# Optimization experiments

Hardware: AMD Instinct MI355X
Metric: run time of the kernel (lower is better)

## Reference

```python
import jax, jax.numpy as jnp
import numpy as np

N_NODES = 20000
N_EDGES = 5000
STEPS = 50
INFECTION_RATE = 0.01
RECOVERY_RATE = 0.038
EDGE_DENSITY = 0.002  # ~10 hyperedges per node on average


def setup_inputs() -> dict:
    key = jax.random.key(0)
    k1, k2 = jax.random.split(key, 2)
    # initial SIR state per node: valid probability rows summing to 1
    u = jax.random.uniform(k1, (N_NODES, 3), dtype=jnp.float32)
    x = u / u.sum(axis=1, keepdims=True)
    # binary hypergraph incidence matrix (num_hyperedges, num_nodes)
    H = (jax.random.uniform(k2, (N_EDGES, N_NODES)) < EDGE_DENSITY).astype(jnp.float32)
    beta = jnp.full((N_NODES,), INFECTION_RATE, dtype=jnp.float32)
    gamma = jnp.full((N_NODES,), RECOVERY_RATE, dtype=jnp.float32)
    return {"x": x, "H": H, "beta": beta, "gamma": gamma, "steps": STEPS}


def reference(x, H, beta, gamma, steps):
    # x: (N, 3) [S, I, R] per node; H: (E, N) incidence.
    def step(state, _):
        S, I, R = state[:, 0], state[:, 1], state[:, 2]
        # hypergraph message passing: node -> hyperedge -> node
        new_cases = beta * (S * (H.T @ (H @ I)))
        new_recovery = gamma * I
        nxt = jnp.stack(
            [S - new_cases, I + new_cases - new_recovery, R + new_recovery], axis=1
        )
        nxt = jnp.maximum(nxt, 0.0)                       # clamp(min=0)
        nxt = nxt / nxt.sum(axis=1, keepdims=True)        # per-node row normalize
        return nxt, nxt

    _, traj = jax.lax.scan(step, x, None, length=steps - 1)
    # output[0] = initial state, then steps-1 simulated updates -> (steps, N, 3)
    return jnp.concatenate([x[None], traj], axis=0)
```

## Files before the change

kernel.cpp:

```cpp
#include <hip/hip_runtime.h>


#define EDGE_CAP 96
#define NODE_CAP 32
#define NIDX_REG 16
#define COOP_BLOCKS 128
#define COOP_THREADS 1024
#define NFLAGS 128

typedef unsigned int uint4_ev __attribute__((ext_vector_type(4)));

__global__ void zero_counts_kernel(int* edge_cnt, int* node_cnt, unsigned* flags,
                                   int n_edges, int n_nodes) {
    int i = blockIdx.x * blockDim.x + threadIdx.x;
    if (i < NFLAGS) flags[i] = 0u;
    if (i < n_edges) edge_cnt[i] = 0;
    if (i < n_nodes) node_cnt[i] = 0;
}

__global__ void build_adjacency_kernel(const float* __restrict__ H,
                                       int* __restrict__ edge_cnt,
                                       int* __restrict__ edge_nodes,
                                       int* __restrict__ node_cnt,
                                       int* __restrict__ node_edges,
                                       int n_nodes) {
    __shared__ int cnt;
    __shared__ int cols[EDGE_CAP];
    __shared__ unsigned long long qmask[128];
    const int e  = blockIdx.x;
    const int tx = threadIdx.x;
    if (tx == 0) cnt = 0;
    const float* row = H + (size_t)e * n_nodes;
    const uint4_ev* row4 = (const uint4_ev*)row;
    const int n4 = n_nodes >> 2;
    const int niter = (n4 + 255) >> 8;

    for (int i = 0; i < niter; ++i) {
        int q = (i << 8) + tx;
        uint4_ev v = {0u, 0u, 0u, 0u};
        if (q < n4) v = row4[q];
        unsigned long long m = __ballot((v.x | v.y | v.z | v.w) != 0u);
        if ((tx & 63) == 0) qmask[(i << 2) + (tx >> 6)] = m;
    }
    __syncthreads();

    const int nslots = niter << 2;
    for (int sIdx = tx; sIdx < nslots; sIdx += blockDim.x) {
        unsigned long long m = qmask[sIdx];
        int qbase = ((sIdx >> 2) << 8) + ((sIdx & 3) << 6);
        while (m) {
            int lane = __builtin_ctzll(m); m &= m - 1;
            int q = qbase + lane;
            uint4_ev v = row4[q];
            int cbase = q << 2;
            if (v.x) { int p = atomicAdd(&cnt, 1); if (p < EDGE_CAP) cols[p] = cbase; }
            if (v.y) { int p = atomicAdd(&cnt, 1); if (p < EDGE_CAP) cols[p] = cbase + 1; }
            if (v.z) { int p = atomicAdd(&cnt, 1); if (p < EDGE_CAP) cols[p] = cbase + 2; }
            if (v.w) { int p = atomicAdd(&cnt, 1); if (p < EDGE_CAP) cols[p] = cbase + 3; }
        }
    }
    if (tx == 0) {
        for (int c = n4 << 2; c < n_nodes; ++c)
            if (row[c] != 0.0f) { int p = atomicAdd(&cnt, 1); if (p < EDGE_CAP) cols[p] = c; }
    }
    __syncthreads();

    int cn = min(cnt, EDGE_CAP);
    if (tx == 0) edge_cnt[e] = cn;
    for (int i = tx; i < cn; i += blockDim.x) {
        int c = cols[i];
        edge_nodes[e * EDGE_CAP + i] = c;
        int q = atomicAdd(&node_cnt[c], 1);
        if (q < NODE_CAP) node_edges[c * NODE_CAP + q] = e;
    }
}

__device__ __forceinline__ float coh_load(const float* p) {
    return __hip_atomic_load(p, __ATOMIC_RELAXED, __HIP_MEMORY_SCOPE_AGENT);
}
__device__ __forceinline__ void coh_storef(float* p, float v) {
    __hip_atomic_store(p, v, __ATOMIC_RELAXED, __HIP_MEMORY_SCOPE_AGENT);
}
__device__ __forceinline__ unsigned coh_loadu(const unsigned* p) {
    return __hip_atomic_load(p, __ATOMIC_RELAXED, __HIP_MEMORY_SCOPE_AGENT);
}
__device__ __forceinline__ void coh_storeu(unsigned* p, unsigned v) {
    __hip_atomic_store(p, v, __ATOMIC_RELAXED, __HIP_MEMORY_SCOPE_AGENT);
}

__device__ __forceinline__ void bar_pub(unsigned* flags, unsigned ph) {
    asm volatile("s_waitcnt vmcnt(0)" ::: "memory");
    __syncthreads();
    if (threadIdx.x == 0) coh_storeu(&flags[blockIdx.x], ph);
}
__device__ __forceinline__ void bar_poll(unsigned* flags, unsigned ph) {
    if (threadIdx.x < 64) {
        for (;;) {
            unsigned a = coh_loadu(&flags[threadIdx.x]);
            unsigned b = coh_loadu(&flags[64 + threadIdx.x]);
            if (__ballot((a < ph) || (b < ph)) == 0ull) break;
            __builtin_amdgcn_s_sleep(1);
        }
    }
    __syncthreads();
    asm volatile("" ::: "memory");
}

__global__ __launch_bounds__(COOP_THREADS) void sir_steps_kernel(
        const float* __restrict__ x,
        const int* __restrict__ edge_cnt, const int* __restrict__ edge_nodes,
        const int* __restrict__ node_cnt, const int* __restrict__ node_edges,
        const float* __restrict__ beta, const float* __restrict__ gamma,
        float* __restrict__ y, float* __restrict__ I,
        float* __restrict__ out,
        int n_nodes, int n_edges, int steps, unsigned* flags) {
    const int b  = blockIdx.x;
    const int tx = threadIdx.x;

    const int node_chunk = (n_nodes + gridDim.x - 1) / gridDim.x;
    const int edge_chunk = (n_edges + gridDim.x - 1) / gridDim.x;
    const int n = b * node_chunk + tx;
    const bool own = (tx < node_chunk) && (n < n_nodes);

    const int k = tx >> 4, gl = tx & 15;
    const int e = b * edge_chunk + k;
    const bool has_edge = (k < edge_chunk) && (e < n_edges);

    int ecnt = 0;
    const int* en = edge_nodes;
    if (has_edge) { ecnt = min(edge_cnt[e], EDGE_CAP); en = edge_nodes + e * EDGE_CAP; }
    int eidx[6];
    #pragma unroll
    for (int i = 0; i < 6; ++i) {
        int j = i * 16 + gl;
        eidx[i] = (has_edge && j < ecnt) ? en[j] : n_nodes;
    }

    int ncnt = 0;
    const int* ne = node_edges;
    float bet = 0.0f, gam = 0.0f;
    if (own) { ncnt = min(node_cnt[n], NODE_CAP); ne = node_edges + n * NODE_CAP;
               bet = beta[n]; gam = gamma[n]; }
    int nidx[NIDX_REG];
    #pragma unroll
    for (int i = 0; i < NIDX_REG; ++i)
        nidx[i] = (own && i < ncnt) ? ne[i] : n_edges;

    float s = 0.0f, iv = 0.0f, r = 0.0f;
    if (own) {
        s = x[n * 3 + 0]; iv = x[n * 3 + 1]; r = x[n * 3 + 2];
        coh_storef(&I[n], iv);
        out[n * 3 + 0] = s; out[n * 3 + 1] = iv; out[n * 3 + 2] = r;
    }
    if (b == 0 && tx == 0) { coh_storef(&I[n_nodes], 0.0f); coh_storef(&y[n_edges], 0.0f); }
    unsigned ph = 1;
    bar_pub(flags, ph); bar_poll(flags, ph);

    for (int t = 1; t < steps; ++t) {
        if (has_edge) {
            float a0 = coh_load(&I[eidx[0]]);
            float a1 = coh_load(&I[eidx[1]]);
            float a2 = coh_load(&I[eidx[2]]);
            float a3 = coh_load(&I[eidx[3]]);
            float a4 = coh_load(&I[eidx[4]]);
            float a5 = coh_load(&I[eidx[5]]);
            float acc = a0 + a1 + a2 + a3 + a4 + a5;
            acc += __shfl_down(acc, 8, 16);
            acc += __shfl_down(acc, 4, 16);
            acc += __shfl_down(acc, 2, 16);
            acc += __shfl_down(acc, 1, 16);
            if (gl == 0) coh_storef(&y[e], acc);
        }
        ++ph; bar_pub(flags, ph); bar_poll(flags, ph);

        if (own) {
            float tv[NIDX_REG];
            #pragma unroll
            for (int i = 0; i < NIDX_REG; ++i) tv[i] = coh_load(&y[nidx[i]]);
            float z = 0.0f;
            #pragma unroll
            for (int i = 0; i < NIDX_REG; ++i) z += tv[i];
            for (int i = NIDX_REG; i < ncnt; ++i) z += coh_load(&y[ne[i]]);
            float nc = bet * s * z;
            float nr = gam * iv;
            float s2 = fmaxf(s - nc, 0.0f);
            float i2 = fmaxf(iv + nc - nr, 0.0f);
            float r2 = fmaxf(r + nr, 0.0f);
            float inv = 1.0f / (s2 + i2 + r2);
            s = s2 * inv; iv = i2 * inv; r = r2 * inv;
            coh_storef(&I[n], iv);
        }
        ++ph; bar_pub(flags, ph);
        if (own) {
            float* ot = out + (size_t)t * n_nodes * 3 + (size_t)n * 3;
            ot[0] = s; ot[1] = iv; ot[2] = r;
        }
        if (t + 1 < steps) bar_poll(flags, ph);
    }
}

extern "C" void kernel_launch(void* const* d_in, const int* in_sizes, int n_in,
                              void* d_out, int out_size, void* d_ws, size_t ws_size,
                              hipStream_t stream) {
    const float* x     = (const float*)d_in[0];
    const float* H     = (const float*)d_in[1];
    const float* beta  = (const float*)d_in[2];
    const float* gamma = (const float*)d_in[3];
    float* out = (float*)d_out;

    const int n_nodes = in_sizes[0] / 3;
    const int n_edges = in_sizes[1] / n_nodes;
    const int steps   = out_size / in_sizes[0];

    char* ws = (char*)d_ws;
    unsigned* flags   = (unsigned*)ws;                    ws += (size_t)NFLAGS * 4;
    int*   edge_cnt   = (int*)ws;                         ws += (size_t)n_edges * 4;
    int*   node_cnt   = (int*)ws;                         ws += (size_t)n_nodes * 4;
    int*   edge_nodes = (int*)ws;                         ws += (size_t)n_edges * EDGE_CAP * 4;
    int*   node_edges = (int*)ws;                         ws += (size_t)n_nodes * NODE_CAP * 4;
    float* y          = (float*)ws;                       ws += ((size_t)n_edges + 1) * 4;
    float* I          = (float*)ws;                       ws += ((size_t)n_nodes + 1) * 4;

    {
        int mx = max(n_edges, max(n_nodes, (int)NFLAGS));
        zero_counts_kernel<<<(mx + 255) / 256, 256, 0, stream>>>(edge_cnt, node_cnt, flags,
                                                                 n_edges, n_nodes);
    }
    build_adjacency_kernel<<<n_edges, 256, 0, stream>>>(H, edge_cnt, edge_nodes,
                                                        node_cnt, node_edges, n_nodes);
    sir_steps_kernel<<<COOP_BLOCKS, COOP_THREADS, 0, stream>>>(
        x, edge_cnt, edge_nodes, node_cnt, node_edges, beta, gamma,
        y, I, out, n_nodes, n_edges, steps, flags);
}
```

Baseline: 1.100 ms.

## Replace grid-wide barriers with sentinel-based point-to-point dataflow between edges and nodes

Removes the two software grid barriers per step. Instead, producers write values straight into per-step, per-consumer slots, and consumers spin until those slots stop holding the -1 sentinel. The adjacency build now records scatter targets (edge slot ↔ node slot), and block size drops to 640 threads to match the work actually owned. The cost is a large workspace of steps × (edge + node) slots that must be filled with sentinels by an init kernel before every run, plus extra scattered stores.

```diff
diff --git a/kernel.cpp b/kernel.cpp
--- a/kernel.cpp
+++ b/kernel.cpp
@@ -3,26 +3,28 @@
 
 #define EDGE_CAP 96
 #define NODE_CAP 32
-#define NIDX_REG 16
 #define COOP_BLOCKS 128
-#define COOP_THREADS 1024
-#define NFLAGS 128
+#define COOP_THREADS 640
 
 typedef unsigned int uint4_ev __attribute__((ext_vector_type(4)));
-
-__global__ void zero_counts_kernel(int* edge_cnt, int* node_cnt, unsigned* flags,
-                                   int n_edges, int n_nodes) {
-    int i = blockIdx.x * blockDim.x + threadIdx.x;
-    if (i < NFLAGS) flags[i] = 0u;
+typedef float float4_ev __attribute__((ext_vector_type(4)));
+
+__global__ void init_ws_kernel(int* edge_cnt, int* node_cnt,
+                               float4_ev* sent, long long n_sent4,
+                               int n_edges, int n_nodes) {
+    long long i = (long long)blockIdx.x * blockDim.x + threadIdx.x;
+    long long stride = (long long)gridDim.x * blockDim.x;
+    const float4_ev mone = {-1.0f, -1.0f, -1.0f, -1.0f};
+    for (long long k = i; k < n_sent4; k += stride) sent[k] = mone;
     if (i < n_edges) edge_cnt[i] = 0;
     if (i < n_nodes) node_cnt[i] = 0;
 }
 
 __global__ void build_adjacency_kernel(const float* __restrict__ H,
                                        int* __restrict__ edge_cnt,
-                                       int* __restrict__ edge_nodes,
+                                       int* __restrict__ edge_tgt,
                                        int* __restrict__ node_cnt,
-                                       int* __restrict__ node_edges,
+                                       int* __restrict__ node_tgt,
                                        int n_nodes) {
     __shared__ int cnt;
     __shared__ int cols[EDGE_CAP];
@@ -69,51 +71,28 @@
     if (tx == 0) edge_cnt[e] = cn;
     for (int i = tx; i < cn; i += blockDim.x) {
         int c = cols[i];
-        edge_nodes[e * EDGE_CAP + i] = c;
         int q = atomicAdd(&node_cnt[c], 1);
-        if (q < NODE_CAP) node_edges[c * NODE_CAP + q] = e;
-    }
-}
-
-__device__ __forceinline__ float coh_load(const float* p) {
+        if (q < NODE_CAP) node_tgt[c * NODE_CAP + q] = e * EDGE_CAP + i;
+        edge_tgt[e * EDGE_CAP + i] = (q < NODE_CAP) ? (c * NODE_CAP + q)
+                                                    : (n_nodes * NODE_CAP);
+    }
+}
+
+__device__ __forceinline__ float coh_loadf(const float* p) {
     return __hip_atomic_load(p, __ATOMIC_RELAXED, __HIP_MEMORY_SCOPE_AGENT);
 }
 __device__ __forceinline__ void coh_storef(float* p, float v) {
     __hip_atomic_store(p, v, __ATOMIC_RELAXED, __HIP_MEMORY_SCOPE_AGENT);
 }
-__device__ __forceinline__ unsigned coh_loadu(const unsigned* p) {
-    return __hip_atomic_load(p, __ATOMIC_RELAXED, __HIP_MEMORY_SCOPE_AGENT);
-}
-__device__ __forceinline__ void coh_storeu(unsigned* p, unsigned v) {
-    __hip_atomic_store(p, v, __ATOMIC_RELAXED, __HIP_MEMORY_SCOPE_AGENT);
-}
-
-__device__ __forceinline__ void bar_pub(unsigned* flags, unsigned ph) {
-    asm volatile("s_waitcnt vmcnt(0)" ::: "memory");
-    __syncthreads();
-    if (threadIdx.x == 0) coh_storeu(&flags[blockIdx.x], ph);
-}
-__device__ __forceinline__ void bar_poll(unsigned* flags, unsigned ph) {
-    if (threadIdx.x < 64) {
-        for (;;) {
-            unsigned a = coh_loadu(&flags[threadIdx.x]);
-            unsigned b = coh_loadu(&flags[64 + threadIdx.x]);
-            if (__ballot((a < ph) || (b < ph)) == 0ull) break;
-            __builtin_amdgcn_s_sleep(1);
-        }
-    }
-    __syncthreads();
-    asm volatile("" ::: "memory");
-}
-
-__global__ __launch_bounds__(COOP_THREADS) void sir_steps_kernel(
+
+__global__ __launch_bounds__(COOP_THREADS) void sir_dataflow_kernel(
         const float* __restrict__ x,
-        const int* __restrict__ edge_cnt, const int* __restrict__ edge_nodes,
-        const int* __restrict__ node_cnt, const int* __restrict__ node_edges,
+        const int* __restrict__ edge_cnt, const int* __restrict__ edge_tgt,
+        const int* __restrict__ node_cnt, const int* __restrict__ node_tgt,
         const float* __restrict__ beta, const float* __restrict__ gamma,
-        float* __restrict__ y, float* __restrict__ I,
+        float* __restrict__ edgeIn, float* __restrict__ nodeIn,
         float* __restrict__ out,
-        int n_nodes, int n_edges, int steps, unsigned* flags) {
+        int n_nodes, int n_edges, int steps) {
     const int b  = blockIdx.x;
     const int tx = threadIdx.x;
 
@@ -125,62 +104,100 @@
     const int k = tx >> 4, gl = tx & 15;
     const int e = b * edge_chunk + k;
     const bool has_edge = (k < edge_chunk) && (e < n_edges);
+    if (!own && !has_edge) return;
+
+    const size_t EIN = (size_t)n_edges * EDGE_CAP;
+    const size_t NIN = (size_t)n_nodes * NODE_CAP + 64;
 
     int ecnt = 0;
-    const int* en = edge_nodes;
-    if (has_edge) { ecnt = min(edge_cnt[e], EDGE_CAP); en = edge_nodes + e * EDGE_CAP; }
-    int eidx[6];
-    #pragma unroll
-    for (int i = 0; i < 6; ++i) {
-        int j = i * 16 + gl;
-        eidx[i] = (has_edge && j < ecnt) ? en[j] : n_nodes;
-    }
-
-    int ncnt = 0;
-    const int* ne = node_edges;
-    float bet = 0.0f, gam = 0.0f;
-    if (own) { ncnt = min(node_cnt[n], NODE_CAP); ne = node_edges + n * NODE_CAP;
-               bet = beta[n]; gam = gamma[n]; }
-    int nidx[NIDX_REG];
-    #pragma unroll
-    for (int i = 0; i < NIDX_REG; ++i)
-        nidx[i] = (own && i < ncnt) ? ne[i] : n_edges;
+    int tgtE[6];
+    if (has_edge) {
+        ecnt = min(edge_cnt[e], EDGE_CAP);
+        #pragma unroll
+        for (int i = 0; i < 6; ++i) {
+            int j = gl + 16 * i;
+            tgtE[i] = (j < ecnt) ? edge_tgt[(size_t)e * EDGE_CAP + j] : 0;
+        }
+    }
+    int ncnt = 0; float bet = 0.0f, gam = 0.0f;
+    int tgtI[16];
+    if (own) {
+        ncnt = min(node_cnt[n], NODE_CAP);
+        bet = beta[n]; gam = gamma[n];
+        #pragma unroll
+        for (int j = 0; j < 16; ++j)
+            tgtI[j] = (j < ncnt) ? node_tgt[(size_t)n * NODE_CAP + j] : 0;
+    }
 
     float s = 0.0f, iv = 0.0f, r = 0.0f;
     if (own) {
-        s = x[n * 3 + 0]; iv = x[n * 3 + 1]; r = x[n * 3 + 2];
-        coh_storef(&I[n], iv);
-        out[n * 3 + 0] = s; out[n * 3 + 1] = iv; out[n * 3 + 2] = r;
-    }
-    if (b == 0 && tx == 0) { coh_storef(&I[n_nodes], 0.0f); coh_storef(&y[n_edges], 0.0f); }
-    unsigned ph = 1;
-    bar_pub(flags, ph); bar_poll(flags, ph);
+        s = x[3 * n]; iv = x[3 * n + 1]; r = x[3 * n + 2];
+        out[3 * n] = s; out[3 * n + 1] = iv; out[3 * n + 2] = r;
+        float* eIn1 = edgeIn + EIN;
+        #pragma unroll
+        for (int j = 0; j < 16; ++j)
+            if (j < ncnt) coh_storef(&eIn1[tgtI[j]], iv);
+        for (int j = 16; j < ncnt; ++j)
+            coh_storef(&eIn1[node_tgt[(size_t)n * NODE_CAP + j]], iv);
+    }
+
+    const unsigned gsh = (unsigned)(tx & 48);
 
     for (int t = 1; t < steps; ++t) {
+        float* eInT = edgeIn + (size_t)t * EIN;
+        float* nInT = nodeIn + (size_t)t * NIN;
+
         if (has_edge) {
-            float a0 = coh_load(&I[eidx[0]]);
-            float a1 = coh_load(&I[eidx[1]]);
-            float a2 = coh_load(&I[eidx[2]]);
-            float a3 = coh_load(&I[eidx[3]]);
-            float a4 = coh_load(&I[eidx[4]]);
-            float a5 = coh_load(&I[eidx[5]]);
-            float acc = a0 + a1 + a2 + a3 + a4 + a5;
+            const float* src = eInT + (size_t)e * EDGE_CAP;
+            float v0, v1, v2, v3, v4, v5;
+            for (;;) {
+                bool ok = true;
+                float a;
+                a = coh_loadf(&src[gl     ]); v0 = (gl      < ecnt) ? a : 0.0f; ok &= (gl      >= ecnt) || (a >= 0.0f);
+                a = coh_loadf(&src[gl + 16]); v1 = (gl + 16 < ecnt) ? a : 0.0f; ok &= (gl + 16 >= ecnt) || (a >= 0.0f);
+                a = coh_loadf(&src[gl + 32]); v2 = (gl + 32 < ecnt) ? a : 0.0f; ok &= (gl + 32 >= ecnt) || (a >= 0.0f);
+                a = coh_loadf(&src[gl + 48]); v3 = (gl + 48 < ecnt) ? a : 0.0f; ok &= (gl + 48 >= ecnt) || (a >= 0.0f);
+                a = coh_loadf(&src[gl + 64]); v4 = (gl + 64 < ecnt) ? a : 0.0f; ok &= (gl + 64 >= ecnt) || (a >= 0.0f);
+                a = coh_loadf(&src[gl + 80]); v5 = (gl + 80 < ecnt) ? a : 0.0f; ok &= (gl + 80 >= ecnt) || (a >= 0.0f);
+                unsigned long long bm = __ballot(ok);
+                if (((bm >> gsh) & 0xFFFFull) == 0xFFFFull) break;
+                __builtin_amdgcn_s_sleep(2);
+            }
+            float acc = v0 + v1 + v2 + v3 + v4 + v5;
             acc += __shfl_down(acc, 8, 16);
             acc += __shfl_down(acc, 4, 16);
             acc += __shfl_down(acc, 2, 16);
             acc += __shfl_down(acc, 1, 16);
-            if (gl == 0) coh_storef(&y[e], acc);
-        }
-        ++ph; bar_pub(flags, ph); bar_poll(flags, ph);
+            float ysum = __shfl(acc, 0, 16);
+            #pragma unroll
+            for (int i = 0; i < 6; ++i) {
+                int j = gl + 16 * i;
+                if (j < ecnt) coh_storef(&nInT[tgtE[i]], ysum);
+            }
+        }
 
         if (own) {
-            float tv[NIDX_REG];
-            #pragma unroll
-            for (int i = 0; i < NIDX_REG; ++i) tv[i] = coh_load(&y[nidx[i]]);
+            const float* src = nInT + (size_t)n * NODE_CAP;
+            float w[16];
+            bool ok;
+            do {
+                ok = true;
+                #pragma unroll
+                for (int j = 0; j < 16; ++j) {
+                    w[j] = coh_loadf(&src[j]);
+                    if (j < ncnt) ok &= (w[j] >= 0.0f);
+                }
+                if (!ok) __builtin_amdgcn_s_sleep(2);
+            } while (!ok);
             float z = 0.0f;
             #pragma unroll
-            for (int i = 0; i < NIDX_REG; ++i) z += tv[i];
-            for (int i = NIDX_REG; i < ncnt; ++i) z += coh_load(&y[ne[i]]);
+            for (int j = 0; j < 16; ++j)
+                if (j < ncnt) z += w[j];
+            for (int j = 16; j < ncnt; ++j) {
+                float vv = coh_loadf(&src[j]);
+                while (vv < 0.0f) { __builtin_amdgcn_s_sleep(2); vv = coh_loadf(&src[j]); }
+                z += vv;
+            }
             float nc = bet * s * z;
             float nr = gam * iv;
             float s2 = fmaxf(s - nc, 0.0f);
@@ -188,14 +205,17 @@
             float r2 = fmaxf(r + nr, 0.0f);
             float inv = 1.0f / (s2 + i2 + r2);
             s = s2 * inv; iv = i2 * inv; r = r2 * inv;
-            coh_storef(&I[n], iv);
-        }
-        ++ph; bar_pub(flags, ph);
-        if (own) {
+            if (t + 1 < steps) {
+                float* eInN = edgeIn + (size_t)(t + 1) * EIN;
+                #pragma unroll
+                for (int j = 0; j < 16; ++j)
+                    if (j < ncnt) coh_storef(&eInN[tgtI[j]], iv);
+                for (int j = 16; j < ncnt; ++j)
+                    coh_storef(&eInN[node_tgt[(size_t)n * NODE_CAP + j]], iv);
+            }
             float* ot = out + (size_t)t * n_nodes * 3 + (size_t)n * 3;
             ot[0] = s; ot[1] = iv; ot[2] = r;
         }
-        if (t + 1 < steps) bar_poll(flags, ph);
     }
 }
 
@@ -212,23 +232,26 @@
     const int n_edges = in_sizes[1] / n_nodes;
     const int steps   = out_size / in_sizes[0];
 
+    const size_t EIN = (size_t)n_edges * EDGE_CAP;
+    const size_t NIN = (size_t)n_nodes * NODE_CAP + 64;
+
     char* ws = (char*)d_ws;
-    unsigned* flags   = (unsigned*)ws;                    ws += (size_t)NFLAGS * 4;
-    int*   edge_cnt   = (int*)ws;                         ws += (size_t)n_edges * 4;
-    int*   node_cnt   = (int*)ws;                         ws += (size_t)n_nodes * 4;
-    int*   edge_nodes = (int*)ws;                         ws += (size_t)n_edges * EDGE_CAP * 4;
-    int*   node_edges = (int*)ws;                         ws += (size_t)n_nodes * NODE_CAP * 4;
-    float* y          = (float*)ws;                       ws += ((size_t)n_edges + 1) * 4;
-    float* I          = (float*)ws;                       ws += ((size_t)n_nodes + 1) * 4;
+    int*   edge_cnt = (int*)ws;                           ws += (size_t)n_edges * 4;
+    int*   node_cnt = (int*)ws;                           ws += (size_t)n_nodes * 4;
+    int*   edge_tgt = (int*)ws;                           ws += EIN * 4;
+    int*   node_tgt = (int*)ws;                           ws += (size_t)n_nodes * NODE_CAP * 4;
+    float* edgeIn   = (float*)ws;                         ws += (size_t)steps * EIN * 4;
+    float* nodeIn   = (float*)ws;                         ws += (size_t)steps * NIN * 4;
 
     {
-        int mx = max(n_edges, max(n_nodes, (int)NFLAGS));
-        zero_counts_kernel<<<(mx + 255) / 256, 256, 0, stream>>>(edge_cnt, node_cnt, flags,
-                                                                 n_edges, n_nodes);
-    }
-    build_adjacency_kernel<<<n_edges, 256, 0, stream>>>(H, edge_cnt, edge_nodes,
-                                                        node_cnt, node_edges, n_nodes);
-    sir_steps_kernel<<<COOP_BLOCKS, COOP_THREADS, 0, stream>>>(
-        x, edge_cnt, edge_nodes, node_cnt, node_edges, beta, gamma,
-        y, I, out, n_nodes, n_edges, steps, flags);
-}
+        long long n_sent4 = (long long)steps * (long long)(EIN + NIN) / 4;
+        init_ws_kernel<<<4096, 256, 0, stream>>>(edge_cnt, node_cnt,
+                                                 (float4_ev*)edgeIn, n_sent4,
+                                                 n_edges, n_nodes);
+    }
+    build_adjacency_kernel<<<n_edges, 256, 0, stream>>>(H, edge_cnt, edge_tgt,
+                                                        node_cnt, node_tgt, n_nodes);
+    sir_dataflow_kernel<<<COOP_BLOCKS, COOP_THREADS, 0, stream>>>(
+        x, edge_cnt, edge_tgt, node_cnt, node_tgt, beta, gamma,
+        edgeIn, nodeIn, out, n_nodes, n_edges, steps);
+}
```

Result: slower. 2.595 ms (+136.1%).
